# Performance work log

Measured on AMD Instinct MI355X. Metric: run time of the kernel, lower is better.

The kernel has to match this reference:

```python
import jax, jax.numpy as jnp
import numpy as np

REFRACTORY_PERIOD = 5
DAMPENING_FACTOR = 0.3


def setup_inputs() -> dict:
    key = jax.random.key(0)
    B, T, N = 32, 4096, 256
    x = jax.random.normal(key, (B, T, N), dtype=jnp.float32)
    return {"x": x}


def _refractory_scan(x):
    # x: [B, T, N]; scan over time keeping refractory counter q resident.
    B, T, N = x.shape
    xt = jnp.swapaxes(x, 0, 1)  # [T, B, N]

    def step(q, x_t):
        cond = (x_t > 0) & (q == 0)
        z_t = jnp.where(cond, jnp.ones_like(q), jnp.zeros_like(q))
        q = jnp.maximum(jnp.zeros_like(q), q - 1) + REFRACTORY_PERIOD * z_t
        return q, z_t

    q0 = jnp.zeros((B, N), dtype=x.dtype)
    # Note: the t=0 case in the original (z0 = x0>0, q = R*z0) is exactly the
    # first step of this scan starting from q0 = 0.
    _, z = jax.lax.scan(step, q0, xt)
    return jnp.swapaxes(z, 0, 1)  # [B, T, N]


def reference(x) -> jnp.ndarray:
    # Forward value is exactly z_forward (the surrogate-gradient straight-through
    # construction leaves the value unchanged).
    return _refractory_scan(x)
```

## Files before the change

### kernel.cpp

```cpp
#include <hip/hip_runtime.h>
#include <cstdint>
#include <cstddef>

#define BB 32
#define TT 4096
#define NNV 64
#define CC 128
#define PSUB 4
#define PG 8
#define MSG_WORDS 32

__global__ __launch_bounds__(256) void refrac_fused(const float* __restrict__ x,
                                                    float* __restrict__ z,
                                                    uint32_t* __restrict__ msg) {
    const int tid = threadIdx.x;
    const int pg = blockIdx.x >> 5;
    const int b  = blockIdx.x & 31;
    const int psub = tid >> 6;
    const int n4 = tid & 63;
    const int p = pg * PSUB + psub;

    const float4* __restrict__ xv = reinterpret_cast<const float4*>(x)
        + ((size_t)b * TT + (size_t)p * CC) * NNV + n4;

    int na[4][6];
    #pragma unroll
    for (int c = 0; c < 4; ++c)
        #pragma unroll
        for (int e = 0; e < 6; ++e) na[c][e] = e;

    uint32_t bits[4][4];

    #pragma unroll
    for (int w = 0; w < 4; ++w) {
        uint32_t cur[4] = {0u, 0u, 0u, 0u};
        for (int jb = 0; jb < 32; jb += 8) {
            float4 buf[8];
            #pragma unroll
            for (int u = 0; u < 8; ++u)
                buf[u] = xv[(size_t)(w * 32 + jb + u) * NNV];
            #pragma unroll
            for (int u = 0; u < 8; ++u) {
                const int j2 = jb + u;
                const int j  = w * 32 + j2;
                const float4 v = buf[u];
                const float fv[4] = {v.x, v.y, v.z, v.w};
                #pragma unroll
                for (int c = 0; c < 4; ++c) {
                    const bool pos = fv[c] > 0.0f;
                    cur[c] |= pos ? (1u << j2) : 0u;
                    #pragma unroll
                    for (int e = 0; e < 6; ++e)
                        if (pos & (j >= na[c][e])) na[c][e] = j + 6;
                }
            }
        }
        #pragma unroll
        for (int c = 0; c < 4; ++c) bits[c][w] = cur[c];
    }

    __shared__ uint32_t tbl_lds[PSUB][256];
    __shared__ uint8_t  ent_lds[PSUB][256];
    __shared__ uint8_t  sout_lds[256];

    #pragma unroll
    for (int c = 0; c < 4; ++c) {
        uint32_t tbl = 0;
        #pragma unroll
        for (int e = 0; e < 6; ++e) {
            int q = na[c][e] - CC;
            q = q > 0 ? q : 0;
            tbl |= (uint32_t)q << (4 * e);
        }
        tbl_lds[psub][n4 * 4 + c] = tbl;
    }
    __syncthreads();

    {
        const int n = tid;
        int e = 0;
        if (pg > 0) {
            const uint32_t* inw = msg + ((size_t)b * PG + (pg - 1)) * MSG_WORDS + (n >> 3);
            uint32_t wv;
            while ((wv = __hip_atomic_load(inw, __ATOMIC_RELAXED,
                                           __HIP_MEMORY_SCOPE_AGENT)) & 0x88888888u)
                __builtin_amdgcn_s_sleep(1);
            e = (int)((wv >> ((n & 7) * 4)) & 0xFu);
        }
        #pragma unroll
        for (int s = 0; s < PSUB; ++s) {
            ent_lds[s][n] = (uint8_t)e;
            e = (int)((tbl_lds[s][n] >> (4 * e)) & 0xFu);
        }
        sout_lds[n] = (uint8_t)e;
    }
    __syncthreads();

    if (pg < PG - 1 && tid < MSG_WORDS) {
        uint32_t wv = 0;
        #pragma unroll
        for (int k = 0; k < 8; ++k)
            wv |= (uint32_t)sout_lds[tid * 8 + k] << (4 * k);
        __hip_atomic_store(msg + ((size_t)b * PG + pg) * MSG_WORDS + tid, wv,
                           __ATOMIC_RELAXED, __HIP_MEMORY_SCOPE_AGENT);
    }

    float4* __restrict__ zv = reinterpret_cast<float4*>(z)
        + ((size_t)b * TT + (size_t)p * CC) * NNV + n4;

    int ea[4];
    #pragma unroll
    for (int c = 0; c < 4; ++c) ea[c] = (int)ent_lds[psub][n4 * 4 + c];

    #pragma unroll
    for (int w = 0; w < 4; ++w) {
        const uint32_t bw[4] = {bits[0][w], bits[1][w], bits[2][w], bits[3][w]};
        for (int j2 = 0; j2 < 32; ++j2) {
            const int j = w * 32 + j2;
            float o[4];
            #pragma unroll
            for (int c = 0; c < 4; ++c) {
                const bool sp = (((bw[c] >> j2) & 1u) != 0u) & (j >= ea[c]);
                if (sp) ea[c] = j + 6;
                o[c] = sp ? 1.0f : 0.0f;
            }
            zv[(size_t)j * NNV] = make_float4(o[0], o[1], o[2], o[3]);
        }
    }
}

extern "C" void kernel_launch(void* const* d_in, const int* in_sizes, int n_in,
                              void* d_out, int out_size, void* d_ws, size_t ws_size,
                              hipStream_t stream) {
    const float* x = (const float*)d_in[0];
    float* z = (float*)d_out;
    uint32_t* msg = (uint32_t*)d_ws;

    hipMemsetAsync(d_ws, 0xAA, (size_t)BB * PG * MSG_WORDS * sizeof(uint32_t), stream);

    refrac_fused<<<dim3(BB * PG), 256, 0, stream>>>(x, z, msg);
}
```

Measured before the change: 245.2 us.

## Split each time chunk into 16 sub-chunks of 32 steps per 1024-thread block

Each block now uses 1024 threads, and each thread handles a 32-step time sub-chunk instead of a 128-step one. This shortens the serial per-thread scan and lets more memory loads be in flight. The bitmask drops to one word per channel, and the entry states are read as one packed word. In exchange, the serial 16-step table composition in the first 256 threads is longer, only a quarter of the threads do that stitching while the rest wait, and register pressure per thread is tighter at the 1024-thread launch bound.

Measured after the change: 235.5 us. 1.04x faster.

```diff
diff --git a/kernel.cpp b/kernel.cpp
--- a/kernel.cpp
+++ b/kernel.cpp
@@ -5,14 +5,14 @@
 #define BB 32
 #define TT 4096
 #define NNV 64
-#define CC 128
-#define PSUB 4
+#define CC 32
+#define PSUB 16
 #define PG 8
 #define MSG_WORDS 32
 
-__global__ __launch_bounds__(256) void refrac_fused(const float* __restrict__ x,
-                                                    float* __restrict__ z,
-                                                    uint32_t* __restrict__ msg) {
+__global__ __launch_bounds__(1024) void refrac_fused(const float* __restrict__ x,
+                                                     float* __restrict__ z,
+                                                     uint32_t* __restrict__ msg) {
     const int tid = threadIdx.x;
     const int pg = blockIdx.x >> 5;
     const int b  = blockIdx.x & 31;
@@ -29,38 +29,31 @@
         #pragma unroll
         for (int e = 0; e < 6; ++e) na[c][e] = e;
 
-    uint32_t bits[4][4];
+    uint32_t cur[4] = {0u, 0u, 0u, 0u};
 
-    #pragma unroll
-    for (int w = 0; w < 4; ++w) {
-        uint32_t cur[4] = {0u, 0u, 0u, 0u};
-        for (int jb = 0; jb < 32; jb += 8) {
-            float4 buf[8];
+    for (int jb = 0; jb < CC; jb += 8) {
+        float4 buf[8];
+        #pragma unroll
+        for (int u = 0; u < 8; ++u)
+            buf[u] = xv[(size_t)(jb + u) * NNV];
+        #pragma unroll
+        for (int u = 0; u < 8; ++u) {
+            const int j = jb + u;
+            const float4 v = buf[u];
+            const float fv[4] = {v.x, v.y, v.z, v.w};
             #pragma unroll
-            for (int u = 0; u < 8; ++u)
-                buf[u] = xv[(size_t)(w * 32 + jb + u) * NNV];
-            #pragma unroll
-            for (int u = 0; u < 8; ++u) {
-                const int j2 = jb + u;
-                const int j  = w * 32 + j2;
-                const float4 v = buf[u];
-                const float fv[4] = {v.x, v.y, v.z, v.w};
+            for (int c = 0; c < 4; ++c) {
+                const bool pos = fv[c] > 0.0f;
+                cur[c] |= pos ? (1u << j) : 0u;
                 #pragma unroll
-                for (int c = 0; c < 4; ++c) {
-                    const bool pos = fv[c] > 0.0f;
-                    cur[c] |= pos ? (1u << j2) : 0u;
-                    #pragma unroll
-                    for (int e = 0; e < 6; ++e)
-                        if (pos & (j >= na[c][e])) na[c][e] = j + 6;
-                }
+                for (int e = 0; e < 6; ++e)
+                    if (pos & (j >= na[c][e])) na[c][e] = j + 6;
             }
         }
-        #pragma unroll
-        for (int c = 0; c < 4; ++c) bits[c][w] = cur[c];
     }
 
     __shared__ uint32_t tbl_lds[PSUB][256];
-    __shared__ uint8_t  ent_lds[PSUB][256];
+    __shared__ uint32_t ent_lds[PSUB][64];
     __shared__ uint8_t  sout_lds[256];
 
     #pragma unroll
@@ -76,7 +69,7 @@
     }
     __syncthreads();
 
-    {
+    if (tid < 256) {
         const int n = tid;
         int e = 0;
         if (pg > 0) {
@@ -89,7 +82,7 @@
         }
         #pragma unroll
         for (int s = 0; s < PSUB; ++s) {
-            ent_lds[s][n] = (uint8_t)e;
+            reinterpret_cast<uint8_t*>(ent_lds[s])[n] = (uint8_t)e;
             e = (int)((tbl_lds[s][n] >> (4 * e)) & 0xFu);
         }
         sout_lds[n] = (uint8_t)e;
@@ -108,24 +101,20 @@
     float4* __restrict__ zv = reinterpret_cast<float4*>(z)
         + ((size_t)b * TT + (size_t)p * CC) * NNV + n4;
 
+    const uint32_t e4 = ent_lds[psub][n4];
     int ea[4];
     #pragma unroll
-    for (int c = 0; c < 4; ++c) ea[c] = (int)ent_lds[psub][n4 * 4 + c];
+    for (int c = 0; c < 4; ++c) ea[c] = (int)((e4 >> (8 * c)) & 0xFFu);
 
-    #pragma unroll
-    for (int w = 0; w < 4; ++w) {
-        const uint32_t bw[4] = {bits[0][w], bits[1][w], bits[2][w], bits[3][w]};
-        for (int j2 = 0; j2 < 32; ++j2) {
-            const int j = w * 32 + j2;
-            float o[4];
-            #pragma unroll
-            for (int c = 0; c < 4; ++c) {
-                const bool sp = (((bw[c] >> j2) & 1u) != 0u) & (j >= ea[c]);
-                if (sp) ea[c] = j + 6;
-                o[c] = sp ? 1.0f : 0.0f;
-            }
-            zv[(size_t)j * NNV] = make_float4(o[0], o[1], o[2], o[3]);
+    for (int j = 0; j < CC; ++j) {
+        float o[4];
+        #pragma unroll
+        for (int c = 0; c < 4; ++c) {
+            const bool sp = (((cur[c] >> j) & 1u) != 0u) & (j >= ea[c]);
+            if (sp) ea[c] = j + 6;
+            o[c] = sp ? 1.0f : 0.0f;
         }
+        zv[(size_t)j * NNV] = make_float4(o[0], o[1], o[2], o[3]);
     }
 }
 
@@ -138,5 +127,5 @@
 
     hipMemsetAsync(d_ws, 0xAA, (size_t)BB * PG * MSG_WORDS * sizeof(uint32_t), stream);
 
-    refrac_fused<<<dim3(BB * PG), 256, 0, stream>>>(x, z, msg);
+    refrac_fused<<<dim3(BB * PG), 1024, 0, stream>>>(x, z, msg);
 }
```
